# Performance work log

Hardware: AMD Instinct MI355X
Metric: run time of the kernel (lower is better)

Reference implementation:

```python
import math
import jax
import jax.numpy as jnp
import numpy as np
from jax import lax

B, IC, OC, K, STYLE_DIM, H, W = 16, 512, 512, 3, 512, 32, 32
EPS = 1e-8


def _blur_kernel():
    # make_kernel([1,3,3,1]) outer product, normalized, times upsample_factor**2 (=4)
    k = jnp.array([1.0, 3.0, 3.0, 1.0], dtype=jnp.float32)
    k2 = k[None, :] * k[:, None]
    k2 = k2 / k2.sum()
    return k2 * 4.0  # [4,4]


def setup_inputs() -> dict:
    key = jax.random.key(0)
    k1, k2, k3, k4 = jax.random.split(key, 4)
    return {
        "input": jax.random.normal(k1, (B, IC, H, W), dtype=jnp.float32),
        "style": jax.random.normal(k2, (B, STYLE_DIM), dtype=jnp.float32),
        "weight": jax.random.normal(k3, (1, OC, IC, K, K), dtype=jnp.float32),
        "mod_weight": jax.random.normal(k4, (IC, STYLE_DIM), dtype=jnp.float32),
        "mod_bias": jnp.ones((IC,), dtype=jnp.float32),  # bias_init=1
    }


def reference(input, style, weight, mod_weight, mod_bias):
    batch, in_ch, h, w_sp = input.shape
    out_ch, ksz = weight.shape[1], weight.shape[3]

    # EqualLinear modulation: scale = 1/sqrt(style_dim), lr_mul=1, no activation
    mod_scale = 1.0 / math.sqrt(mod_weight.shape[1])
    s = style @ (mod_weight * mod_scale).T + mod_bias  # [B, IC]

    # modulate + demodulate
    conv_scale = 1.0 / math.sqrt(in_ch * ksz * ksz)
    wmod = conv_scale * weight * s[:, None, :, None, None]  # [B, OC, IC, K, K]
    demod = lax.rsqrt(jnp.sum(wmod * wmod, axis=(2, 3, 4)) + EPS)  # [B, OC]
    wmod = wmod * demod[:, :, None, None, None]

    # conv_transpose2d(stride=2, padding=0, groups=batch) == per-sample conv with
    # lhs_dilation=2, full padding (K-1), spatially flipped kernel in OIHW layout.
    w_conv = wmod[:, :, :, ::-1, ::-1]  # [B, OC, IC, K, K]

    def one_sample(x, wk):
        # x: [IC, H, W], wk: [OC, IC, K, K] -> [OC, 2H+K-2+1, ...] (65x65 here)
        return lax.conv_general_dilated(
            x[None], wk, window_strides=(1, 1),
            padding=[(ksz - 1, ksz - 1)] * 2,
            lhs_dilation=(2, 2),
            dimension_numbers=("NCHW", "OIHW", "NCHW"))[0]

    out = jax.vmap(one_sample)(input, w_conv)  # [B, OC, 65, 65]

    # Blur: upfirdn2d(up=1, down=1, pad=(1,1)) with symmetric 4x4 kernel -> depthwise conv
    bk = _blur_kernel()
    out = jnp.pad(out, ((0, 0), (0, 0), (1, 1), (1, 1)))
    dk = jnp.tile(bk[None, None], (out_ch, 1, 1, 1))  # [OC, 1, 4, 4]
    out = lax.conv_general_dilated(
        out, dk, window_strides=(1, 1), padding="VALID",
        feature_group_count=out_ch,
        dimension_numbers=("NCHW", "OIHW", "NCHW"))  # [B, OC, 64, 64]
    return out
```

## Files before the change

kernel.cpp:

```cpp
#include <hip/hip_runtime.h>
#include <stdint.h>

typedef unsigned int uint32;
typedef unsigned short u16;
typedef short short8 __attribute__((ext_vector_type(8)));
typedef float floatx4 __attribute__((ext_vector_type(4)));

#define OFF_S      0u
#define OFF_DS     32768u
#define OFF_WSUM   65536u
#define OFF_WPACK  1114112u
#define OFF_XST    5832704u
#define OFF_U      22609920u

__device__ __forceinline__ u16 f2bf(float x){
    uint32 u = __float_as_uint(x);
    uint32 r = (u + 0x7FFFu + ((u>>16)&1u)) >> 16;
    return (u16)r;
}
__device__ __forceinline__ float bf2f(u16 h){
    return __uint_as_float(((uint32)h)<<16);
}

#define GLL16(gp, lp) \
    __builtin_amdgcn_global_load_lds( \
        (const __attribute__((address_space(1))) void*)(gp), \
        (__attribute__((address_space(3))) void*)(lp), 16, 0, 0)

__global__ __launch_bounds__(256) void k_style(const float* __restrict__ style,
                                               const float* __restrict__ mw,
                                               const float* __restrict__ mb,
                                               float* __restrict__ s){
    int gid = blockIdx.x*4 + (threadIdx.x>>6);
    int lane = threadIdx.x & 63;
    int b = gid>>9, ic = gid & 511;
    const float* sp = style + b*512;
    const float* wp = mw + (size_t)ic*512;
    float acc = 0.f;
    for (int d=lane; d<512; d+=64) acc += sp[d]*wp[d];
    for (int off=32; off; off>>=1) acc += __shfl_down(acc, off, 64);
    if (lane==0) s[b*512+ic] = acc*0.044194173824159216f + mb[ic];
}

__global__ __launch_bounds__(256) void k_wprep(const float* __restrict__ w,
                                               float* __restrict__ wsum,
                                               u16* __restrict__ wp){
    int idx = blockIdx.x*256 + threadIdx.x;
    const float* p = w + (size_t)idx*9;
    float vv[9]; float a = 0.f;
    #pragma unroll
    for (int t=0;t<9;++t){ float v=p[t]; vv[t]=v; a += v*v; }
    wsum[idx] = a;
    #pragma unroll
    for (int t=0;t<9;++t) wp[(size_t)t*262144 + idx] = f2bf(vv[t]);
}

__global__ __launch_bounds__(256) void k_dscale(const float* __restrict__ s,
                                                const float* __restrict__ wsum,
                                                float* __restrict__ ds){
    int gid = blockIdx.x*4 + (threadIdx.x>>6);
    int lane = threadIdx.x & 63;
    int b = gid>>9, oc = gid & 511;
    const float* sp = s + b*512;
    const float* wp = wsum + (size_t)oc*512;
    float acc=0.f;
    for (int d=lane; d<512; d+=64){ float sv = sp[d]; acc += sv*sv*wp[d]; }
    for (int off=32; off; off>>=1) acc += __shfl_down(acc, off, 64);
    if (lane==0){
        const float cs = 0.014731391274719738f;
        ds[b*512+oc] = cs * rsqrtf(cs*cs*acc + 1e-8f);
    }
}

__global__ __launch_bounds__(256) void k_xst(const float* __restrict__ in,
                                             const float* __restrict__ s,
                                             u16* __restrict__ xst){
    int bx = blockIdx.x;
    int b = bx>>5, i = bx&31;
    __shared__ u16 tr[32*520];
    int tid = threadIdx.x;
    int j = tid & 31;
    for (int ic = tid>>5; ic < 512; ic += 8){
        float v = in[((size_t)(b*512+ic)*32 + i)*32 + j] * s[b*512+ic];
        tr[j*520 + ic] = f2bf(v);
    }
    __syncthreads();
    for (int v = tid; v < 2048; v += 256){
        int jj = v>>6, ic8 = (v&63)*8;
        *(uint4*)(xst + (size_t)(b*1024 + i*32 + jj)*512 + ic8) =
            *(const uint4*)(&tr[jj*520 + ic8]);
    }
}

__global__ __launch_bounds__(256) void k_gemm(const u16* __restrict__ A,
                                              const u16* __restrict__ Bx,
                                              u16* __restrict__ C,
                                              int Ncols){
    int n0 = blockIdx.x * 128;
    int m0 = blockIdx.y * 128;
    int tid = threadIdx.x, lane = tid & 63, w = tid >> 6;
    int wm = w>>1, wn = w&1;
    int np = lane & 15, qq = lane >> 4;

    __shared__ __align__(16) char smem[32768];
    u16* Asm = (u16*)smem;
    u16* Bsm = (u16*)(smem + 16384);
    u16* Csm = (u16*)smem;

    int rsub = lane >> 3;
    int gsw  = (lane & 7) ^ rsub;

    floatx4 acc[4][4] = {};

    for (int k0 = 0; k0 < 512; k0 += 64){
        #pragma unroll
        for (int q = 0; q < 4; ++q){
            int row = q*32 + w*8 + rsub;
            GLL16(A + (size_t)(m0+row)*512 + k0 + gsw*8, &Asm[(q*32 + w*8)*64]);
        }
        #pragma unroll
        for (int q = 0; q < 4; ++q){
            int row = q*32 + w*8 + rsub;
            GLL16(Bx + (size_t)(n0+row)*512 + k0 + gsw*8, &Bsm[(q*32 + w*8)*64]);
        }
        __syncthreads();
        #pragma unroll
        for (int kk = 0; kk < 2; ++kk){
            short8 af[4], bfr[4];
            #pragma unroll
            for (int mf = 0; mf < 4; ++mf){
                int row = wm*64 + mf*16 + np;
                int gs = (kk*4 + qq) ^ (np & 7);
                af[mf] = *(const short8*)(&Asm[row*64 + gs*8]);
            }
            #pragma unroll
            for (int nf = 0; nf < 4; ++nf){
                int row = wn*64 + nf*16 + np;
                int gs = (kk*4 + qq) ^ (np & 7);
                bfr[nf] = *(const short8*)(&Bsm[row*64 + gs*8]);
            }
            #pragma unroll
            for (int mf = 0; mf < 4; ++mf)
                #pragma unroll
                for (int nf = 0; nf < 4; ++nf)
                    acc[mf][nf] = __builtin_amdgcn_mfma_f32_16x16x32_bf16(
                        af[mf], bfr[nf], acc[mf][nf], 0,0,0);
        }
        __syncthreads();
    }
    #pragma unroll
    for (int mf = 0; mf < 4; ++mf){
        #pragma unroll
        for (int reg = 0; reg < 4; ++reg){
            int row = wm*64 + mf*16 + qq*4 + reg;
            #pragma unroll
            for (int nf = 0; nf < 4; ++nf){
                int col = wn*64 + nf*16 + np;
                int c = col >> 3;
                Csm[row*128 + ((c ^ (row & 15)) << 3) + (col & 7)] =
                    f2bf(acc[mf][nf][reg]);
            }
        }
    }
    __syncthreads();
    {
        int c = tid & 15;
        #pragma unroll
        for (int it = 0; it < 8; ++it){
            int row = it*16 + (tid >> 4);
            uint4 v = *(const uint4*)(&Csm[row*128 + ((c ^ (row & 15)) << 3)]);
            *(uint4*)(C + (size_t)(m0+row)*Ncols + n0 + c*8) = v;
        }
    }
}

__global__ __launch_bounds__(256) void k_blur2(const u16* __restrict__ U,
                                               const float* __restrict__ ds,
                                               float* __restrict__ out,
                                               int b0, int Ncols){
    int oc = blockIdx.x;
    int bp = blockIdx.y;
    int b  = b0 + bp;
    __shared__ __align__(16) u16 Usm[9*1024];
    __shared__ __align__(16) u16 HRsm[3*32*64];
    int tid = threadIdx.x;

    const u16* src0 = U + (size_t)oc*Ncols + (size_t)bp*1024;
    size_t tapstride = (size_t)512 * Ncols;
    #pragma unroll
    for (int it = 0; it < 5; ++it){
        int i = tid + it*256;
        if (i < 1152){
            int tap = i>>7, c8 = i & 127;
            *(uint4*)(&Usm[tap*1024 + c8*8]) =
                *(const uint4*)(src0 + tap*tapstride + c8*8);
        }
    }
    __syncthreads();

    #pragma unroll
    for (int it = 0; it < 12; ++it){
        int task = tid + it*256;
        int a = task >> 10, rem = task & 1023;
        int i = rem >> 5, u = rem & 31;
        const u16* base = Usm + a*3072 + i*32;
        float u0  = bf2f(base[u]);
        float u1  = bf2f(base[1024 + u]);
        float u2  = bf2f(base[2048 + u]);
        float u0p = (u < 31) ? bf2f(base[u + 1])        : 0.f;
        float u1m = (u > 0)  ? bf2f(base[1024 + u - 1]) : 0.f;
        float u1p = (u < 31) ? bf2f(base[1024 + u + 1]) : 0.f;
        float u2m = (u > 0)  ? bf2f(base[2048 + u - 1]) : 0.f;
        float HRe = u1m + 3.f*(u0 + u2m + u1) + u0p + u2;
        float HRo = u0 + u2m + 3.f*(u1 + u0p + u2) + u1p;
        uint32 packed = (uint32)f2bf(HRe) | ((uint32)f2bf(HRo) << 16);
        *(uint32*)(&HRsm[(a*32 + i)*64 + 2*u]) = packed;
    }
    __syncthreads();

    float dsc = ds[b*512 + oc] * (1.f/16.f);
    float* op = out + (size_t)(b*512 + oc) * 4096;
    #pragma unroll
    for (int it = 0; it < 4; ++it){
        int task = tid + it*256;
        int Y = task >> 4, X0 = (task & 15) * 4;
        float o0=0.f,o1=0.f,o2=0.f,o3=0.f;
        int v = Y >> 1;
        #define ACCROW(aa, ii, ww) do{ \
            int _i = (ii); \
            if ((unsigned)_i < 32u){ \
                uint2 rv = *(const uint2*)(&HRsm[((aa)*32 + _i)*64 + X0]); \
                o0 += (ww)*__uint_as_float((rv.x & 0xffffu) << 16); \
                o1 += (ww)*__uint_as_float(rv.x & 0xffff0000u); \
                o2 += (ww)*__uint_as_float((rv.y & 0xffffu) << 16); \
                o3 += (ww)*__uint_as_float(rv.y & 0xffff0000u); \
            } }while(0)
        if ((Y & 1) == 0){
            ACCROW(1, v-1, 1.f);
            ACCROW(0, v,   3.f);
            ACCROW(2, v-1, 3.f);
            ACCROW(1, v,   3.f);
            ACCROW(0, v+1, 1.f);
            ACCROW(2, v,   1.f);
        } else {
            ACCROW(0, v,   1.f);
            ACCROW(2, v-1, 1.f);
            ACCROW(1, v,   3.f);
            ACCROW(0, v+1, 3.f);
            ACCROW(2, v,   3.f);
            ACCROW(1, v+1, 1.f);
        }
        #undef ACCROW
        float4 res = make_float4(dsc*o0, dsc*o1, dsc*o2, dsc*o3);
        *(float4*)(op + Y*64 + X0) = res;
    }
}

extern "C" void kernel_launch(void* const* d_in, const int* in_sizes, int n_in,
                              void* d_out, int out_size, void* d_ws, size_t ws_size,
                              hipStream_t stream){
    const float* input  = (const float*)d_in[0];
    const float* style  = (const float*)d_in[1];
    const float* weight = (const float*)d_in[2];
    const float* mw     = (const float*)d_in[3];
    const float* mb     = (const float*)d_in[4];
    float* out = (float*)d_out;
    char* ws = (char*)d_ws;
    float* s     = (float*)(ws + OFF_S);
    float* ds    = (float*)(ws + OFF_DS);
    float* wsum  = (float*)(ws + OFF_WSUM);
    u16*   wpack = (u16*)(ws + OFF_WPACK);
    u16*   xst   = (u16*)(ws + OFF_XST);
    u16*   U     = (u16*)(ws + OFF_U);

    int NB;
    if      (ws_size >= (size_t)OFF_U + (size_t)4608*16384*2) NB = 16;
    else if (ws_size >= (size_t)OFF_U + (size_t)4608*8192*2)  NB = 8;
    else                                                       NB = 4;
    int npass = 16 / NB;
    int Ncols = NB * 1024;

    k_style <<<2048, 256, 0, stream>>>(style, mw, mb, s);
    k_wprep <<<1024, 256, 0, stream>>>(weight, wsum, wpack);
    k_dscale<<<2048, 256, 0, stream>>>(s, wsum, ds);
    k_xst   <<<512,  256, 0, stream>>>(input, s, xst);

    for (int p = 0; p < npass; ++p){
        const u16* xp = xst + (size_t)p * NB * 1024 * 512;
        k_gemm <<<dim3(Ncols/128, 36), 256, 0, stream>>>(wpack, xp, U, Ncols);
        k_blur2<<<dim3(512, NB),       256, 0, stream>>>(U, ds, out, p*NB, Ncols);
    }
}
```

Measured before the change: 319.5 us.

## Rewrite GEMM with 256x256 tiles, 4-stage LDS pipeline and swizzled grid

```diff
diff --git a/kernel.cpp b/kernel.cpp
--- a/kernel.cpp
+++ b/kernel.cpp
@@ -92,85 +92,100 @@
     }
 }
 
-__global__ __launch_bounds__(256) void k_gemm(const u16* __restrict__ A,
-                                              const u16* __restrict__ Bx,
-                                              u16* __restrict__ C,
-                                              int Ncols){
-    int n0 = blockIdx.x * 128;
-    int m0 = blockIdx.y * 128;
-    int tid = threadIdx.x, lane = tid & 63, w = tid >> 6;
-    int wm = w>>1, wn = w&1;
+__global__ __launch_bounds__(512, 2) void k_gemm(const u16* __restrict__ A,
+                                                 const u16* __restrict__ Bx,
+                                                 u16* __restrict__ C,
+                                                 int Ncols){
+    int cpx = gridDim.x >> 3;
+    int bid = blockIdx.x;
+    int swz = (bid & 7)*cpx + (bid >> 3);
+    int bx = swz / 18;
+    int by = swz - bx*18;
+    int m0 = by*256, n0 = bx*256;
+
+    int tid = threadIdx.x;
+    int lane = tid & 63;
+    int w  = tid >> 6;
+    int wm = w >> 2, wn = w & 3;
     int np = lane & 15, qq = lane >> 4;
 
-    __shared__ __align__(16) char smem[32768];
-    u16* Asm = (u16*)smem;
-    u16* Bsm = (u16*)(smem + 16384);
+    __shared__ __align__(16) char smem[131072];
+
+    int c1 = tid,      r1 = c1 >> 2, s1 = c1 & 3, g1 = s1 ^ ((r1 >> 1) & 3);
+    int c2 = tid + 512, r2 = c2 >> 2, s2 = c2 & 3, g2 = s2 ^ ((r2 >> 1) & 3);
+    const u16* srcA1 = A  + (size_t)(m0 + r1)*512 + g1*8;
+    const u16* srcA2 = A  + (size_t)(m0 + r2)*512 + g2*8;
+    const u16* srcB1 = Bx + (size_t)(n0 + r1)*512 + g1*8;
+    const u16* srcB2 = Bx + (size_t)(n0 + r2)*512 + g2*8;
+    int offA1 = (tid & ~63)*8;
+    int offA2 = offA1 + 4096;
+
+    #define STAGE(T) do{ \
+        u16* _b = (u16*)smem + ((T)&3)*16384; \
+        GLL16(srcA1 + (size_t)(T)*32, _b + offA1); \
+        GLL16(srcA2 + (size_t)(T)*32, _b + offA2); \
+        GLL16(srcB1 + (size_t)(T)*32, _b + 8192 + offA1); \
+        GLL16(srcB2 + (size_t)(T)*32, _b + 8192 + offA2); \
+    }while(0)
+
+    int sA = (qq ^ ((np >> 1) & 3)) * 8;
+    int pAoff = (wm*128 + np)*32 + sA;
+    int pBoff = (wn*64  + np)*32 + sA;
+
+    floatx4 acc[8][4] = {};
+
+    STAGE(0); STAGE(1); STAGE(2);
+    asm volatile("s_waitcnt vmcnt(8)" ::: "memory");
+    __builtin_amdgcn_s_barrier();
+
+    #pragma unroll
+    for (int t = 0; t < 16; ++t){
+        const u16* base = (const u16*)smem + (t & 3)*16384;
+        short8 af[8], bfr[4];
+        #pragma unroll
+        for (int mf = 0; mf < 8; ++mf)
+            af[mf] = *(const short8*)(base + pAoff + mf*512);
+        #pragma unroll
+        for (int nf = 0; nf < 4; ++nf)
+            bfr[nf] = *(const short8*)(base + 8192 + pBoff + nf*512);
+
+        if (t < 13) STAGE(t+3);
+
+        __builtin_amdgcn_s_setprio(1);
+        #pragma unroll
+        for (int mf = 0; mf < 8; ++mf)
+            #pragma unroll
+            for (int nf = 0; nf < 4; ++nf)
+                acc[mf][nf] = __builtin_amdgcn_mfma_f32_16x16x32_bf16(
+                    af[mf], bfr[nf], acc[mf][nf], 0,0,0);
+        __builtin_amdgcn_s_setprio(0);
+
+        if      (t < 13)  asm volatile("s_waitcnt vmcnt(8)" ::: "memory");
+        else if (t == 13) asm volatile("s_waitcnt vmcnt(4)" ::: "memory");
+        else if (t == 14) asm volatile("s_waitcnt vmcnt(0)" ::: "memory");
+        __builtin_amdgcn_s_barrier();
+    }
+    #undef STAGE
+
     u16* Csm = (u16*)smem;
-
-    int rsub = lane >> 3;
-    int gsw  = (lane & 7) ^ rsub;
-
-    floatx4 acc[4][4] = {};
-
-    for (int k0 = 0; k0 < 512; k0 += 64){
+    #pragma unroll
+    for (int mf = 0; mf < 8; ++mf){
+        int row0 = wm*128 + mf*16 + qq*4;
         #pragma unroll
-        for (int q = 0; q < 4; ++q){
-            int row = q*32 + w*8 + rsub;
-            GLL16(A + (size_t)(m0+row)*512 + k0 + gsw*8, &Asm[(q*32 + w*8)*64]);
+        for (int nf = 0; nf < 4; ++nf){
+            int col = wn*64 + nf*16 + np;
+            #pragma unroll
+            for (int reg = 0; reg < 4; ++reg)
+                Csm[(row0+reg)*256 + col] = f2bf(acc[mf][nf][reg]);
         }
-        #pragma unroll
-        for (int q = 0; q < 4; ++q){
-            int row = q*32 + w*8 + rsub;
-            GLL16(Bx + (size_t)(n0+row)*512 + k0 + gsw*8, &Bsm[(q*32 + w*8)*64]);
-        }
-        __syncthreads();
-        #pragma unroll
-        for (int kk = 0; kk < 2; ++kk){
-            short8 af[4], bfr[4];
-            #pragma unroll
-            for (int mf = 0; mf < 4; ++mf){
-                int row = wm*64 + mf*16 + np;
-                int gs = (kk*4 + qq) ^ (np & 7);
-                af[mf] = *(const short8*)(&Asm[row*64 + gs*8]);
-            }
-            #pragma unroll
-            for (int nf = 0; nf < 4; ++nf){
-                int row = wn*64 + nf*16 + np;
-                int gs = (kk*4 + qq) ^ (np & 7);
-                bfr[nf] = *(const short8*)(&Bsm[row*64 + gs*8]);
-            }
-            #pragma unroll
-            for (int mf = 0; mf < 4; ++mf)
-                #pragma unroll
-                for (int nf = 0; nf < 4; ++nf)
-                    acc[mf][nf] = __builtin_amdgcn_mfma_f32_16x16x32_bf16(
-                        af[mf], bfr[nf], acc[mf][nf], 0,0,0);
-        }
-        __syncthreads();
-    }
-    #pragma unroll
-    for (int mf = 0; mf < 4; ++mf){
-        #pragma unroll
-        for (int reg = 0; reg < 4; ++reg){
-            int row = wm*64 + mf*16 + qq*4 + reg;
-            #pragma unroll
-            for (int nf = 0; nf < 4; ++nf){
-                int col = wn*64 + nf*16 + np;
-                int c = col >> 3;
-                Csm[row*128 + ((c ^ (row & 15)) << 3) + (col & 7)] =
-                    f2bf(acc[mf][nf][reg]);
-            }
-        }
     }
     __syncthreads();
-    {
-        int c = tid & 15;
-        #pragma unroll
-        for (int it = 0; it < 8; ++it){
-            int row = it*16 + (tid >> 4);
-            uint4 v = *(const uint4*)(&Csm[row*128 + ((c ^ (row & 15)) << 3)]);
-            *(uint4*)(C + (size_t)(m0+row)*Ncols + n0 + c*8) = v;
-        }
+    #pragma unroll
+    for (int i = 0; i < 16; ++i){
+        int c = tid + i*512;
+        int row = c >> 5, cc = c & 31;
+        uint4 v = *(const uint4*)(&Csm[row*256 + cc*8]);
+        *(uint4*)(C + (size_t)(m0+row)*Ncols + n0 + cc*8) = v;
     }
 }
 
@@ -279,6 +294,7 @@
     else                                                       NB = 4;
     int npass = 16 / NB;
     int Ncols = NB * 1024;
+    int nTilesN = Ncols / 256;
 
     k_style <<<2048, 256, 0, stream>>>(style, mw, mb, s);
     k_wprep <<<1024, 256, 0, stream>>>(weight, wsum, wpack);
@@ -287,7 +303,7 @@
 
     for (int p = 0; p < npass; ++p){
         const u16* xp = xst + (size_t)p * NB * 1024 * 512;
-        k_gemm <<<dim3(Ncols/128, 36), 256, 0, stream>>>(wpack, xp, U, Ncols);
+        k_gemm <<<dim3(18*nTilesN), 512, 0, stream>>>(wpack, xp, U, Ncols);
         k_blur2<<<dim3(512, NB),       256, 0, stream>>>(U, ds, out, p*NB, Ncols);
     }
 }
```

New measurement: 338.2 us. 5.8% more time.
